# Kernel tuning notes

Measured on AMD Instinct MI355X. Metric: run time of the kernel, lower is better.

## Reference

```python
import jax, jax.numpy as jnp
import numpy as np

N = 10000      # nodes
E = 100000     # edges
H = 256        # hidden_dim
HEADS = 4
HD = H // HEADS
G = 8          # graphs in batch
SPG = N // G   # nodes per graph (equal-size graphs -> to_dense_batch is a reshape)
IN = 16        # in_dim
PE = 5         # pe_dims
ED = 8         # edge_dim
OUT = 4        # out_dim
L = 5          # num_layers


def setup_inputs() -> dict:
    key = jax.random.key(0)
    ks = iter(jax.random.split(key, 64))
    rn = lambda shape, s=0.05: jax.random.normal(next(ks), shape, jnp.float32) * s
    inp = {}
    inp['x'] = jax.random.normal(next(ks), (N, IN), jnp.float32)
    inp['pe'] = jax.random.normal(next(ks), (N, PE), jnp.float32)
    inp['edge_attr'] = jax.random.normal(next(ks), (E, ED), jnp.float32)
    inp['edge_index'] = jax.random.randint(next(ks), (2, E), 0, N, jnp.int32)
    inp['batch'] = (jnp.arange(N) // SPG).astype(jnp.int32)
    # node encoders (3 node types), stacked
    inp['enc_w1'] = rn((3, IN + PE, H)); inp['enc_b1'] = rn((3, H))
    inp['enc_w2'] = rn((3, H, H));       inp['enc_b2'] = rn((3, H))
    # edge encoder
    inp['ee_w1'] = rn((ED, H)); inp['ee_b1'] = rn((H,))
    inp['ee_w2'] = rn((H, H));  inp['ee_b2'] = rn((H,))
    # per-layer edge / node update MLPs, stacked over layers
    inp['eu_w1'] = rn((L, 3 * H, H)); inp['eu_b1'] = rn((L, H))
    inp['eu_w2'] = rn((L, H, H));     inp['eu_b2'] = rn((L, H))
    inp['nu_w1'] = rn((L, 2 * H, H)); inp['nu_b1'] = rn((L, H))
    inp['nu_w2'] = rn((L, H, H));     inp['nu_b2'] = rn((L, H))
    # MultiheadAttention (combined in-proj + out-proj)
    inp['qkv_w'] = rn((H, 3 * H)); inp['qkv_b'] = rn((3 * H,))
    inp['out_w'] = rn((H, H));     inp['out_b'] = rn((H,))
    # fusion MLP
    inp['fu_w1'] = rn((H, H)); inp['fu_b1'] = rn((H,))
    inp['fu_w2'] = rn((H, H)); inp['fu_b2'] = rn((H,))
    # decoders (3 node types)
    inp['dec_w1'] = rn((3, H, H));   inp['dec_b1'] = rn((3, H))
    inp['dec_w2'] = rn((3, H, OUT)); inp['dec_b2'] = rn((3, OUT))
    return inp


def _mlp(z, w1, b1, w2, b2):
    return jnp.maximum(z @ w1 + b1, 0.0) @ w2 + b2


def reference(x, pe, edge_attr, edge_index, batch,
              enc_w1, enc_b1, enc_w2, enc_b2,
              ee_w1, ee_b1, ee_w2, ee_b2,
              eu_w1, eu_b1, eu_w2, eu_b2,
              nu_w1, nu_b1, nu_w2, nu_b2,
              qkv_w, qkv_b, out_w, out_b,
              fu_w1, fu_b1, fu_w2, fu_b2,
              dec_w1, dec_b1, dec_w2, dec_b2):
    n = x.shape[0]
    node_types = (jnp.clip(jnp.round(x[:, 2] * 3.0), 1.0, 3.0).astype(jnp.int32) - 1)
    rng_n = jnp.arange(n)

    # node encoding: run all 3 type-MLPs, select per node (masked dispatch in torch)
    inp = jnp.concatenate([x, pe], axis=-1)                       # [N, IN+PE]
    hid = jnp.maximum(jnp.einsum('ni,tih->tnh', inp, enc_w1) + enc_b1[:, None, :], 0.0)
    h_all = jnp.einsum('tnh,tho->tno', hid, enc_w2) + enc_b2[:, None, :]  # [3,N,H]
    h_nodes = h_all[node_types, rng_n]                            # [N, H]

    h_edges = _mlp(edge_attr, ee_w1, ee_b1, ee_w2, ee_b2)         # [E, H]

    src, dst = edge_index[0], edge_index[1]
    for l in range(L):
        e_in = jnp.concatenate([h_nodes[src], h_nodes[dst], h_edges], axis=-1)  # [E,3H]
        h_edges = h_edges + _mlp(e_in, eu_w1[l], eu_b1[l], eu_w2[l], eu_b2[l])
        m_node = jax.ops.segment_sum(h_edges, dst, num_segments=n)              # index_add_
        n_in = jnp.concatenate([h_nodes, m_node], axis=-1)                      # [N,2H]
        h_nodes = h_nodes + _mlp(n_in, nu_w1[l], nu_b1[l], nu_w2[l], nu_b2[l])

    # global attention: equal-size graphs -> to_dense_batch is a reshape, mask all-true
    xp = h_nodes.reshape(G, SPG, H)
    qkv = xp @ qkv_w + qkv_b                                      # [G,S,3H]
    q, k, v = jnp.split(qkv, 3, axis=-1)
    split_heads = lambda t: t.reshape(G, SPG, HEADS, HD).transpose(0, 2, 1, 3)
    q, k, v = split_heads(q), split_heads(k), split_heads(v)
    scale = 1.0 / np.sqrt(HD).astype(np.float32)
    att = jax.nn.softmax(jnp.einsum('ghsd,ghtd->ghst', q, k) * scale, axis=-1)
    o = jnp.einsum('ghst,ghtd->ghsd', att, v).transpose(0, 2, 1, 3).reshape(G, SPG, H)
    glob = (xp + (o @ out_w + out_b)).reshape(n, H)

    h = _mlp(h_nodes + glob, fu_w1, fu_b1, fu_w2, fu_b2)

    dhid = jnp.maximum(jnp.einsum('nh,tho->tno', h, dec_w1) + dec_b1[:, None, :], 0.0)
    out_all = jnp.einsum('tno,tok->tnk', dhid, dec_w2) + dec_b2[:, None, :]     # [3,N,OUT]
    return out_all[node_types, rng_n]
```

## Files before the change

kernel.cpp:

```cpp
#include <hip/hip_runtime.h>
#include <hip/hip_bf16.h>
#include <math.h>

#define NN 10000
#define NE 100000
#define SPGc 1250
#define NG 8
#define NL 5
#define ECHK 25000

__device__ __forceinline__ int imin(int a, int b) { return a < b ? a : b; }

__global__ __launch_bounds__(256) void k_types(const float* __restrict__ x, int* __restrict__ types) {
    int i = blockIdx.x * 256 + threadIdx.x;
    if (i < NN) {
        float v = rintf(x[(size_t)i * 16 + 2] * 3.0f);
        v = fminf(fmaxf(v, 1.0f), 3.0f);
        types[i] = (int)v - 1;
    }
}

__global__ __launch_bounds__(256) void k_hist(const int* __restrict__ dst, int* __restrict__ deg) {
    int e = blockIdx.x * 256 + threadIdx.x;
    if (e < NE) atomicAdd(&deg[dst[e]], 1);
}

__global__ __launch_bounds__(256) void k_scan(const int* __restrict__ deg, int* __restrict__ row_ptr,
                                              int* __restrict__ cursor) {
    __shared__ int buf[256];
    int tid = threadIdx.x;
    int base = 0;
    for (int c = 0; c < NN; c += 256) {
        int i = c + tid;
        int v = (i < NN) ? deg[i] : 0;
        buf[tid] = v;
        __syncthreads();
        for (int off = 1; off < 256; off <<= 1) {
            int t = (tid >= off) ? buf[tid - off] : 0;
            __syncthreads();
            buf[tid] += t;
            __syncthreads();
        }
        if (i < NN) {
            row_ptr[i + 1] = base + buf[tid];
            cursor[i] = base + buf[tid] - v;
        }
        __syncthreads();
        base += buf[255];
        __syncthreads();
    }
    if (tid == 0) row_ptr[0] = 0;
}

__global__ __launch_bounds__(256) void k_scatter(const int* __restrict__ dst, int* __restrict__ cursor,
                                                 int* __restrict__ csr) {
    int e = blockIdx.x * 256 + threadIdx.x;
    if (e < NE) {
        int p = atomicAdd(&cursor[dst[e]], 1);
        csr[p] = e;
    }
}

__global__ __launch_bounds__(256) void k_enc(const float* __restrict__ x, const float* __restrict__ pe,
        const int* __restrict__ types,
        const float* __restrict__ w1, const float* __restrict__ b1,
        const float* __restrict__ w2, const float* __restrict__ b2,
        float* __restrict__ h_nodes) {
    int n = blockIdx.x;
    int j = threadIdx.x;
    __shared__ float inp[21];
    __shared__ float hid[256];
    if (j < 16) inp[j] = x[(size_t)n * 16 + j];
    else if (j < 21) inp[j] = pe[(size_t)n * 5 + (j - 16)];
    __syncthreads();
    int t = types[n];
    const float* W1 = w1 + (size_t)t * 21 * 256;
    float a = b1[t * 256 + j];
    #pragma unroll
    for (int i = 0; i < 21; ++i) a = fmaf(inp[i], W1[i * 256 + j], a);
    hid[j] = fmaxf(a, 0.f);
    __syncthreads();
    const float* W2 = w2 + (size_t)t * 256 * 256;
    float o = b2[t * 256 + j];
    for (int k = 0; k < 256; ++k) o = fmaf(hid[k], W2[k * 256 + j], o);
    h_nodes[(size_t)n * 256 + j] = o;
}

__global__ __launch_bounds__(256) void gemm64(int Mrows, int K, int Nout,
        const float* __restrict__ A0, int lda,
        const float* __restrict__ W, const float* __restrict__ bias,
        float* __restrict__ C) {
    __shared__ __align__(16) float As[16][68];
    __shared__ __align__(16) float Ws[16][64];
    int tid = threadIdx.x;
    int tx = tid & 15, ty = tid >> 4;
    int blockRow = blockIdx.x * 64;
    int ncol0 = blockIdx.y * 64;
    float acc[4][4];
    #pragma unroll
    for (int i = 0; i < 4; ++i)
        #pragma unroll
        for (int j = 0; j < 4; ++j) acc[i][j] = 0.f;

    for (int k0 = 0; k0 < K; k0 += 16) {
        #pragma unroll
        for (int i = 0; i < 4; ++i) {
            int id = tid + 256 * i;
            int kk = id & 15, r = id >> 4;
            int grow = blockRow + r;
            int k = k0 + kk;
            float v = 0.f;
            if (grow < Mrows && k < K) v = A0[(size_t)grow * lda + k];
            As[kk][r] = v;
        }
        #pragma unroll
        for (int i = 0; i < 4; ++i) {
            int id = tid + 256 * i;
            int c = id & 63, kk = id >> 6;
            int k = k0 + kk;
            Ws[kk][c] = (k < K) ? W[(size_t)k * Nout + ncol0 + c] : 0.f;
        }
        __syncthreads();
        #pragma unroll
        for (int kk = 0; kk < 16; ++kk) {
            const float4 a4 = *(const float4*)&As[kk][ty << 2];
            const float4 w4 = *(const float4*)&Ws[kk][tx << 2];
            float av[4] = {a4.x, a4.y, a4.z, a4.w};
            float wv[4] = {w4.x, w4.y, w4.z, w4.w};
            #pragma unroll
            for (int i = 0; i < 4; ++i)
                #pragma unroll
                for (int j = 0; j < 4; ++j)
                    acc[i][j] = fmaf(av[i], wv[j], acc[i][j]);
        }
        __syncthreads();
    }
    #pragma unroll
    for (int i = 0; i < 4; ++i) {
        int grow = blockRow + (ty << 2) + i;
        if (grow >= Mrows) continue;
        size_t base = (size_t)grow * Nout + ncol0 + (tx << 2);
        #pragma unroll
        for (int j = 0; j < 4; ++j)
            C[base + j] = fmaxf(acc[i][j] + bias[ncol0 + (tx << 2) + j], 0.f);
    }
}

template<int AMODE, bool RELU, bool HASRES, bool PGATH, bool HASBIAS>
__global__ __launch_bounds__(256) void gemm_f32(int Mrows, int K, int Nout,
        const float* __restrict__ A0, const float* __restrict__ A1, int lda, int rowOfsA,
        const int* __restrict__ gsrc, const int* __restrict__ gdst,
        const float* __restrict__ Pa, const float* __restrict__ Pb,
        const float* __restrict__ W, const float* __restrict__ bias,
        const float* __restrict__ ResF, float resScale, int rowOfsC,
        float* __restrict__ C) {
    __shared__ __align__(16) float As[16][68];
    __shared__ __align__(16) float Ws[16][16][20];
    int tid = threadIdx.x;
    int blockRow = blockIdx.x * 64;
    int ncol0 = blockIdx.y * 256;
    int r4 = tid >> 4, c16 = tid & 15;
    int sar = tid >> 2, sak = (tid & 3) * 4;
    int swk = tid >> 4, scg = tid & 15;
    float acc[4][16];
    #pragma unroll
    for (int i = 0; i < 4; ++i)
        #pragma unroll
        for (int n = 0; n < 16; ++n) acc[i][n] = 0.f;

    for (int k0 = 0; k0 < K; k0 += 16) {
        {
            int arow = imin(blockRow + sar, Mrows - 1) + rowOfsA;
            float4 av;
            if (AMODE == 0) {
                av = *(const float4*)(A0 + (size_t)arow * lda + k0 + sak);
            } else {
                int k = k0 + sak;
                av = (k < 256) ? *(const float4*)(A0 + (size_t)arow * 256 + k)
                               : *(const float4*)(A1 + (size_t)arow * 256 + (k - 256));
            }
            As[sak + 0][sar] = av.x;
            As[sak + 1][sar] = av.y;
            As[sak + 2][sar] = av.z;
            As[sak + 3][sar] = av.w;
        }
        {
            const float* wp = W + (size_t)(k0 + swk) * Nout + ncol0 + scg * 16;
            *(float4*)&Ws[swk][scg][0]  = *(const float4*)(wp + 0);
            *(float4*)&Ws[swk][scg][4]  = *(const float4*)(wp + 4);
            *(float4*)&Ws[swk][scg][8]  = *(const float4*)(wp + 8);
            *(float4*)&Ws[swk][scg][12] = *(const float4*)(wp + 12);
        }
        __syncthreads();
        #pragma unroll
        for (int kk = 0; kk < 16; ++kk) {
            const float4 a4 = *(const float4*)&As[kk][r4 << 2];
            float av[4] = {a4.x, a4.y, a4.z, a4.w};
            #pragma unroll
            for (int q = 0; q < 4; ++q) {
                const float4 w4 = *(const float4*)&Ws[kk][c16][q << 2];
                float wv[4] = {w4.x, w4.y, w4.z, w4.w};
                #pragma unroll
                for (int i = 0; i < 4; ++i)
                    #pragma unroll
                    for (int j = 0; j < 4; ++j)
                        acc[i][q * 4 + j] = fmaf(av[i], wv[j], acc[i][q * 4 + j]);
            }
        }
        __syncthreads();
    }
    #pragma unroll
    for (int i = 0; i < 4; ++i) {
        int grow = blockRow + (r4 << 2) + i;
        if (grow >= Mrows) continue;
        size_t crow = (size_t)(grow + rowOfsC);
        int colb = ncol0 + (c16 << 4);
        const float* par = nullptr;
        const float* pbr = nullptr;
        if (PGATH) {
            int e = grow + rowOfsA;
            par = Pa + (size_t)gsrc[e] * 256 + colb;
            pbr = Pb + (size_t)gdst[e] * 256 + colb;
        }
        #pragma unroll
        for (int q = 0; q < 4; ++q) {
            float v[4];
            #pragma unroll
            for (int j = 0; j < 4; ++j) v[j] = acc[i][q * 4 + j];
            if (HASBIAS) {
                const float4 b4 = *(const float4*)(bias + colb + q * 4);
                v[0] += b4.x; v[1] += b4.y; v[2] += b4.z; v[3] += b4.w;
            }
            if (PGATH) {
                const float4 pa4 = *(const float4*)(par + q * 4);
                const float4 pb4 = *(const float4*)(pbr + q * 4);
                v[0] += pa4.x + pb4.x; v[1] += pa4.y + pb4.y;
                v[2] += pa4.z + pb4.z; v[3] += pa4.w + pb4.w;
            }
            if (RELU) {
                v[0] = fmaxf(v[0], 0.f); v[1] = fmaxf(v[1], 0.f);
                v[2] = fmaxf(v[2], 0.f); v[3] = fmaxf(v[3], 0.f);
            }
            if (HASRES) {
                const float4 rv = *(const float4*)(ResF + crow * Nout + colb + q * 4);
                v[0] += resScale * rv.x; v[1] += resScale * rv.y;
                v[2] += resScale * rv.z; v[3] += resScale * rv.w;
            }
            float4 o; o.x = v[0]; o.y = v[1]; o.z = v[2]; o.w = v[3];
            *(float4*)(C + crow * Nout + colb + q * 4) = o;
        }
    }
}

__global__ __launch_bounds__(256) void k_mnode(const float* __restrict__ h_edges,
        const int* __restrict__ row_ptr, const int* __restrict__ csr, float* __restrict__ m_node) {
    int n = blockIdx.x * 4 + (threadIdx.x >> 6);
    int lane = threadIdx.x & 63;
    if (n >= NN) return;
    float a0 = 0.f, a1 = 0.f, a2 = 0.f, a3 = 0.f;
    int s = row_ptr[n], e = row_ptr[n + 1];
    for (int i = s; i < e; ++i) {
        int ed = csr[i];
        const float4 v = *(const float4*)(h_edges + (size_t)ed * 256 + (lane << 2));
        a0 += v.x; a1 += v.y; a2 += v.z; a3 += v.w;
    }
    float4 r; r.x = a0; r.y = a1; r.z = a2; r.w = a3;
    *(float4*)(m_node + (size_t)n * 256 + (lane << 2)) = r;
}

__global__ __launch_bounds__(256) void k_attn(const float* __restrict__ qkv, float* __restrict__ obuf) {
    int gh = blockIdx.y;
    int g = gh >> 2, h = gh & 3;
    int q0 = blockIdx.x * 64;
    int tid = threadIdx.x;
    int r = tid >> 2, q4 = tid & 3;
    int d0 = q4 * 16;
    __shared__ __align__(16) float Ks[32][64];
    __shared__ __align__(16) float Vs[32][64];
    const float* base = qkv + (size_t)g * SPGc * 768;
    int my_s = q0 + r;
    bool rowok = my_s < SPGc;
    float qreg[16];
    #pragma unroll
    for (int dd = 0; dd < 16; ++dd) qreg[dd] = 0.f;
    if (rowok) {
        const float* qp = base + (size_t)my_s * 768 + h * 64 + d0;
        #pragma unroll
        for (int dd = 0; dd < 16; ++dd) qreg[dd] = qp[dd];
    }
    float m = -1e30f, l = 0.f;
    float oacc[16];
    #pragma unroll
    for (int dd = 0; dd < 16; ++dd) oacc[dd] = 0.f;

    for (int t0 = 0; t0 < SPGc; t0 += 32) {
        #pragma unroll
        for (int i = 0; i < 8; ++i) {
            int id = tid + 256 * i;
            int d = id & 63, jj = id >> 6;
            int s = t0 + jj;
            float kv = 0.f, vv = 0.f;
            if (s < SPGc) {
                const float* kp = base + (size_t)s * 768 + h * 64;
                kv = kp[256 + d];
                vv = kp[512 + d];
            }
            Ks[jj][d] = kv;
            Vs[jj][d] = vv;
        }
        __syncthreads();
        float sc[32];
        #pragma unroll
        for (int j = 0; j < 32; ++j) {
            float p = 0.f;
            #pragma unroll
            for (int dd = 0; dd < 16; dd += 4) {
                const float4 k4 = *(const float4*)&Ks[j][d0 + dd];
                p = fmaf(qreg[dd], k4.x, p);
                p = fmaf(qreg[dd + 1], k4.y, p);
                p = fmaf(qreg[dd + 2], k4.z, p);
                p = fmaf(qreg[dd + 3], k4.w, p);
            }
            sc[j] = p;
        }
        #pragma unroll
        for (int j = 0; j < 32; ++j) {
            float p = sc[j];
            p += __shfl_xor(p, 1);
            p += __shfl_xor(p, 2);
            sc[j] = (t0 + j < SPGc) ? p * 0.125f : -1e30f;
        }
        float mt = sc[0];
        #pragma unroll
        for (int j = 1; j < 32; ++j) mt = fmaxf(mt, sc[j]);
        float mnew = fmaxf(m, mt);
        float f = __expf(m - mnew);
        l *= f;
        #pragma unroll
        for (int dd = 0; dd < 16; ++dd) oacc[dd] *= f;
        #pragma unroll
        for (int j = 0; j < 32; ++j) {
            float p = __expf(sc[j] - mnew);
            l += p;
            #pragma unroll
            for (int dd = 0; dd < 16; dd += 4) {
                const float4 v4 = *(const float4*)&Vs[j][d0 + dd];
                oacc[dd]     = fmaf(p, v4.x, oacc[dd]);
                oacc[dd + 1] = fmaf(p, v4.y, oacc[dd + 1]);
                oacc[dd + 2] = fmaf(p, v4.z, oacc[dd + 2]);
                oacc[dd + 3] = fmaf(p, v4.w, oacc[dd + 3]);
            }
        }
        m = mnew;
        __syncthreads();
    }
    if (rowok) {
        float rinv = 1.0f / l;
        float* op = obuf + (size_t)(g * SPGc + my_s) * 256 + h * 64 + d0;
        #pragma unroll
        for (int dd = 0; dd < 16; ++dd) op[dd] = oacc[dd] * rinv;
    }
}

__global__ __launch_bounds__(256) void k_dec(const float* __restrict__ h, const int* __restrict__ types,
        const float* __restrict__ w1, const float* __restrict__ b1,
        const float* __restrict__ w2, const float* __restrict__ b2,
        float* __restrict__ out) {
    int n = blockIdx.x;
    int j = threadIdx.x;
    __shared__ float hrow[256];
    __shared__ float dhid[256];
    hrow[j] = h[(size_t)n * 256 + j];
    __syncthreads();
    int t = types[n];
    const float* W1 = w1 + (size_t)t * 256 * 256;
    float a = b1[t * 256 + j];
    for (int k = 0; k < 256; ++k) a = fmaf(hrow[k], W1[k * 256 + j], a);
    dhid[j] = fmaxf(a, 0.f);
    __syncthreads();
    int lane = j & 63, w = j >> 6;
    const float* W2 = w2 + (size_t)t * 256 * 4;
    float p = 0.f;
    #pragma unroll
    for (int q = 0; q < 4; ++q) {
        int kk = lane + 64 * q;
        p = fmaf(dhid[kk], W2[kk * 4 + w], p);
    }
    #pragma unroll
    for (int o2 = 32; o2 > 0; o2 >>= 1) p += __shfl_down(p, o2);
    if (lane == 0) out[(size_t)n * 4 + w] = p + b2[t * 4 + w];
}

extern "C" void kernel_launch(void* const* d_in, const int* in_sizes, int n_in,
                              void* d_out, int out_size, void* d_ws, size_t ws_size,
                              hipStream_t stream) {
    const float* x         = (const float*)d_in[0];
    const float* pe        = (const float*)d_in[1];
    const float* edge_attr = (const float*)d_in[2];
    const int*   eidx      = (const int*)d_in[3];
    const float* enc_w1 = (const float*)d_in[5];
    const float* enc_b1 = (const float*)d_in[6];
    const float* enc_w2 = (const float*)d_in[7];
    const float* enc_b2 = (const float*)d_in[8];
    const float* ee_w1  = (const float*)d_in[9];
    const float* ee_b1  = (const float*)d_in[10];
    const float* ee_w2  = (const float*)d_in[11];
    const float* ee_b2  = (const float*)d_in[12];
    const float* eu_w1  = (const float*)d_in[13];
    const float* eu_b1  = (const float*)d_in[14];
    const float* eu_w2  = (const float*)d_in[15];
    const float* eu_b2  = (const float*)d_in[16];
    const float* nu_w1  = (const float*)d_in[17];
    const float* nu_b1  = (const float*)d_in[18];
    const float* nu_w2  = (const float*)d_in[19];
    const float* nu_b2  = (const float*)d_in[20];
    const float* qkv_w  = (const float*)d_in[21];
    const float* qkv_b  = (const float*)d_in[22];
    const float* out_w  = (const float*)d_in[23];
    const float* out_b  = (const float*)d_in[24];
    const float* fu_w1  = (const float*)d_in[25];
    const float* fu_b1  = (const float*)d_in[26];
    const float* fu_w2  = (const float*)d_in[27];
    const float* fu_b2  = (const float*)d_in[28];
    const float* dec_w1 = (const float*)d_in[29];
    const float* dec_b1 = (const float*)d_in[30];
    const float* dec_w2 = (const float*)d_in[31];
    const float* dec_b2 = (const float*)d_in[32];

    const int* src  = eidx;
    const int* dstp = eidx + NE;

    float* ws = (float*)d_ws;
    float* h_edges = ws;
    float* big     = ws + 25600000;
    float* h_nodes = ws + 37120000;
    float* mn_ob   = ws + 39680000;
    float* nhid    = ws + 42240000;
    int* ibase   = (int*)(ws + 44800000);
    int* types   = ibase;
    int* deg     = ibase + NN;
    int* row_ptr = deg + NN;
    int* cursor  = row_ptr + NN + 1;
    int* csr     = cursor + NN;

    float* ehid = big;
    float* Pa   = big + 6400000;
    float* Pb   = big + 8960000;
    float* qkvf = big;
    float* fin  = big + 7680000;

    hipMemsetAsync(deg, 0, NN * sizeof(int), stream);
    k_types<<<(NN + 255) / 256, 256, 0, stream>>>(x, types);
    k_hist<<<(NE + 255) / 256, 256, 0, stream>>>(dstp, deg);
    k_scan<<<1, 256, 0, stream>>>(deg, row_ptr, cursor);
    k_scatter<<<(NE + 255) / 256, 256, 0, stream>>>(dstp, cursor, csr);

    k_enc<<<NN, 256, 0, stream>>>(x, pe, types, enc_w1, enc_b1, enc_w2, enc_b2, h_nodes);

    dim3 gE((ECHK + 63) / 64, 1);
    dim3 gN((NN + 63) / 64, 1);

    for (int c0 = 0; c0 < NE; c0 += ECHK) {
        gemm64<<<dim3((ECHK + 63) / 64, 4), 256, 0, stream>>>(ECHK, 8, 256,
            edge_attr + (size_t)c0 * 8, 8, ee_w1, ee_b1, ehid);
        gemm_f32<0, false, false, false, true><<<gE, 256, 0, stream>>>(ECHK, 256, 256,
            ehid, nullptr, 256, 0, nullptr, nullptr, nullptr, nullptr,
            ee_w2, ee_b2, nullptr, 0.f, c0, h_edges);
    }

    for (int l = 0; l < NL; ++l) {
        const float* W1 = eu_w1 + (size_t)l * 768 * 256;
        gemm_f32<0, false, false, false, false><<<gN, 256, 0, stream>>>(NN, 256, 256,
            h_nodes, nullptr, 256, 0, nullptr, nullptr, nullptr, nullptr,
            W1, nullptr, nullptr, 0.f, 0, Pa);
        gemm_f32<0, false, false, false, false><<<gN, 256, 0, stream>>>(NN, 256, 256,
            h_nodes, nullptr, 256, 0, nullptr, nullptr, nullptr, nullptr,
            W1 + 65536, nullptr, nullptr, 0.f, 0, Pb);
        for (int c0 = 0; c0 < NE; c0 += ECHK) {
            gemm_f32<0, true, false, true, true><<<gE, 256, 0, stream>>>(ECHK, 256, 256,
                h_edges, nullptr, 256, c0, src, dstp, Pa, Pb,
                W1 + 131072, eu_b1 + l * 256, nullptr, 0.f, 0, ehid);
            gemm_f32<0, false, true, false, true><<<gE, 256, 0, stream>>>(ECHK, 256, 256,
                ehid, nullptr, 256, 0, nullptr, nullptr, nullptr, nullptr,
                eu_w2 + (size_t)l * 65536, eu_b2 + l * 256, h_edges, 1.f, c0, h_edges);
        }
        k_mnode<<<(NN + 3) / 4, 256, 0, stream>>>(h_edges, row_ptr, csr, mn_ob);
        gemm_f32<2, true, false, false, true><<<gN, 256, 0, stream>>>(NN, 512, 256,
            h_nodes, mn_ob, 256, 0, nullptr, nullptr, nullptr, nullptr,
            nu_w1 + (size_t)l * 131072, nu_b1 + l * 256, nullptr, 0.f, 0, nhid);
        gemm_f32<0, false, true, false, true><<<gN, 256, 0, stream>>>(NN, 256, 256,
            nhid, nullptr, 256, 0, nullptr, nullptr, nullptr, nullptr,
            nu_w2 + (size_t)l * 65536, nu_b2 + l * 256, h_nodes, 1.f, 0, h_nodes);
    }

    gemm_f32<0, false, false, false, true><<<dim3((NN + 63) / 64, 3), 256, 0, stream>>>(NN, 256, 768,
        h_nodes, nullptr, 256, 0, nullptr, nullptr, nullptr, nullptr,
        qkv_w, qkv_b, nullptr, 0.f, 0, qkvf);

    dim3 ga((SPGc + 63) / 64, NG * 4);
    k_attn<<<ga, 256, 0, stream>>>(qkvf, mn_ob);

    gemm_f32<0, false, true, false, true><<<gN, 256, 0, stream>>>(NN, 256, 256,
        mn_ob, nullptr, 256, 0, nullptr, nullptr, nullptr, nullptr,
        out_w, out_b, h_nodes, 2.f, 0, fin);
    gemm_f32<0, true, false, false, true><<<gN, 256, 0, stream>>>(NN, 256, 256,
        fin, nullptr, 256, 0, nullptr, nullptr, nullptr, nullptr,
        fu_w1, fu_b1, nullptr, 0.f, 0, nhid);
    gemm_f32<0, false, false, false, true><<<gN, 256, 0, stream>>>(NN, 256, 256,
        nhid, nullptr, 256, 0, nullptr, nullptr, nullptr, nullptr,
        fu_w2, fu_b2, nullptr, 0.f, 0, mn_ob);

    k_dec<<<NN, 256, 0, stream>>>(mn_ob, types, dec_w1, dec_b1, dec_w2, dec_b2, (float*)d_out);
}
```

Before: 4.436 ms.

## Fuse edge MLP into one kernel keeping hidden tile in LDS, narrow node GEMM tiles

```diff
diff --git a/kernel.cpp b/kernel.cpp
--- a/kernel.cpp
+++ b/kernel.cpp
@@ -7,7 +7,6 @@
 #define SPGc 1250
 #define NG 8
 #define NL 5
-#define ECHK 25000
 
 __device__ __forceinline__ int imin(int a, int b) { return a < b ? a : b; }
 
@@ -82,95 +81,165 @@
     __syncthreads();
     const float* W2 = w2 + (size_t)t * 256 * 256;
     float o = b2[t * 256 + j];
+    #pragma unroll 8
     for (int k = 0; k < 256; ++k) o = fmaf(hid[k], W2[k * 256 + j], o);
     h_nodes[(size_t)n * 256 + j] = o;
 }
 
-__global__ __launch_bounds__(256) void gemm64(int Mrows, int K, int Nout,
-        const float* __restrict__ A0, int lda,
+template<bool GATHER, bool RES>
+__global__ __launch_bounds__(256) void k_eu(int Mrows, int K1,
+        const float* __restrict__ A, int lda,
+        const float* __restrict__ W1, const float* __restrict__ b1,
+        const int* __restrict__ gs, const int* __restrict__ gd,
+        const float* __restrict__ Pa, const float* __restrict__ Pb,
+        const float* __restrict__ W2, const float* __restrict__ b2,
+        float* __restrict__ HE) {
+    __shared__ __align__(16) float E[256][65];
+    __shared__ __align__(16) float As[8][68];
+    __shared__ __align__(16) float Ws[8][16][20];
+    int tid = threadIdx.x;
+    int blockRow = blockIdx.x * 64;
+    int rg = tid >> 4, cg = tid & 15;
+    float acc[4][16];
+    #pragma unroll
+    for (int i = 0; i < 4; ++i)
+        #pragma unroll
+        for (int n = 0; n < 16; ++n) acc[i][n] = 0.f;
+
+    for (int k0 = 0; k0 < K1; k0 += 8) {
+        {
+            int row = tid & 63, kh = tid >> 6;
+            int arow = imin(blockRow + row, Mrows - 1);
+            const float* ap = A + (size_t)arow * lda + k0 + kh * 2;
+            float2 a2 = *(const float2*)ap;
+            As[kh * 2][row] = a2.x;
+            As[kh * 2 + 1][row] = a2.y;
+        }
+        {
+            int kk = tid >> 5, cgw = (tid >> 1) & 15, half = tid & 1;
+            const float* wp = W1 + (size_t)(k0 + kk) * 256 + cgw * 16 + half * 8;
+            float4 w0 = *(const float4*)wp;
+            float4 w1 = *(const float4*)(wp + 4);
+            *(float4*)&Ws[kk][cgw][half * 8]     = w0;
+            *(float4*)&Ws[kk][cgw][half * 8 + 4] = w1;
+        }
+        __syncthreads();
+        #pragma unroll
+        for (int kk = 0; kk < 8; ++kk) {
+            const float4 a4 = *(const float4*)&As[kk][rg << 2];
+            float av[4] = {a4.x, a4.y, a4.z, a4.w};
+            #pragma unroll
+            for (int q = 0; q < 4; ++q) {
+                const float4 w4 = *(const float4*)&Ws[kk][cg][q << 2];
+                float wv[4] = {w4.x, w4.y, w4.z, w4.w};
+                #pragma unroll
+                for (int i = 0; i < 4; ++i)
+                    #pragma unroll
+                    for (int j = 0; j < 4; ++j)
+                        acc[i][q * 4 + j] = fmaf(av[i], wv[j], acc[i][q * 4 + j]);
+            }
+        }
+        __syncthreads();
+    }
+    int gsi[4], gdi[4];
+    if (GATHER) {
+        #pragma unroll
+        for (int i = 0; i < 4; ++i) {
+            int e = imin(blockRow + (rg << 2) + i, Mrows - 1);
+            gsi[i] = gs[e];
+            gdi[i] = gd[e];
+        }
+    }
+    #pragma unroll
+    for (int n = 0; n < 16; ++n) {
+        int col = (cg << 4) + n;
+        float bv = b1[col];
+        float4 w;
+        float* wf = (float*)&w;
+        #pragma unroll
+        for (int i = 0; i < 4; ++i) {
+            float v = acc[i][n] + bv;
+            if (GATHER) v += Pa[(size_t)gsi[i] * 256 + col] + Pb[(size_t)gdi[i] * 256 + col];
+            wf[i] = fmaxf(v, 0.f);
+        }
+        *(float4*)&E[col][rg << 2] = w;
+    }
+    #pragma unroll
+    for (int i = 0; i < 4; ++i)
+        #pragma unroll
+        for (int n = 0; n < 16; ++n) acc[i][n] = 0.f;
+    __syncthreads();
+
+    for (int k0 = 0; k0 < 256; k0 += 8) {
+        {
+            int kk = tid >> 5, cgw = (tid >> 1) & 15, half = tid & 1;
+            const float* wp = W2 + (size_t)(k0 + kk) * 256 + cgw * 16 + half * 8;
+            float4 w0 = *(const float4*)wp;
+            float4 w1 = *(const float4*)(wp + 4);
+            *(float4*)&Ws[kk][cgw][half * 8]     = w0;
+            *(float4*)&Ws[kk][cgw][half * 8 + 4] = w1;
+        }
+        __syncthreads();
+        #pragma unroll
+        for (int kk = 0; kk < 8; ++kk) {
+            const float4 a4 = *(const float4*)&E[k0 + kk][rg << 2];
+            float av[4] = {a4.x, a4.y, a4.z, a4.w};
+            #pragma unroll
+            for (int q = 0; q < 4; ++q) {
+                const float4 w4 = *(const float4*)&Ws[kk][cg][q << 2];
+                float wv[4] = {w4.x, w4.y, w4.z, w4.w};
+                #pragma unroll
+                for (int i = 0; i < 4; ++i)
+                    #pragma unroll
+                    for (int j = 0; j < 4; ++j)
+                        acc[i][q * 4 + j] = fmaf(av[i], wv[j], acc[i][q * 4 + j]);
+            }
+        }
+        __syncthreads();
+    }
+    #pragma unroll
+    for (int i = 0; i < 4; ++i) {
+        int row = blockRow + (rg << 2) + i;
+        if (row >= Mrows) continue;
+        size_t base = (size_t)row * 256 + (cg << 4);
+        #pragma unroll
+        for (int q = 0; q < 4; ++q) {
+            const float4 b4 = *(const float4*)(b2 + (cg << 4) + q * 4);
+            float v[4] = {acc[i][q * 4 + 0] + b4.x, acc[i][q * 4 + 1] + b4.y,
+                          acc[i][q * 4 + 2] + b4.z, acc[i][q * 4 + 3] + b4.w};
+            if (RES) {
+                const float4 rv = *(const float4*)(HE + base + q * 4);
+                v[0] += rv.x; v[1] += rv.y; v[2] += rv.z; v[3] += rv.w;
+            }
+            float4 o; o.x = v[0]; o.y = v[1]; o.z = v[2]; o.w = v[3];
+            *(float4*)(HE + base + q * 4) = o;
+        }
+    }
+}
+
+template<int AMODE, bool RELU, bool HASRES, bool HASBIAS>
+__global__ __launch_bounds__(256) void gemm_f32(int Mrows, int K, int Nout,
+        const float* __restrict__ A0, const float* __restrict__ A1, int lda,
         const float* __restrict__ W, const float* __restrict__ bias,
+        const float* __restrict__ ResF, float resScale,
         float* __restrict__ C) {
     __shared__ __align__(16) float As[16][68];
-    __shared__ __align__(16) float Ws[16][64];
-    int tid = threadIdx.x;
-    int tx = tid & 15, ty = tid >> 4;
-    int blockRow = blockIdx.x * 64;
-    int ncol0 = blockIdx.y * 64;
-    float acc[4][4];
-    #pragma unroll
-    for (int i = 0; i < 4; ++i)
-        #pragma unroll
-        for (int j = 0; j < 4; ++j) acc[i][j] = 0.f;
-
-    for (int k0 = 0; k0 < K; k0 += 16) {
-        #pragma unroll
-        for (int i = 0; i < 4; ++i) {
-            int id = tid + 256 * i;
-            int kk = id & 15, r = id >> 4;
-            int grow = blockRow + r;
-            int k = k0 + kk;
-            float v = 0.f;
-            if (grow < Mrows && k < K) v = A0[(size_t)grow * lda + k];
-            As[kk][r] = v;
-        }
-        #pragma unroll
-        for (int i = 0; i < 4; ++i) {
-            int id = tid + 256 * i;
-            int c = id & 63, kk = id >> 6;
-            int k = k0 + kk;
-            Ws[kk][c] = (k < K) ? W[(size_t)k * Nout + ncol0 + c] : 0.f;
-        }
-        __syncthreads();
-        #pragma unroll
-        for (int kk = 0; kk < 16; ++kk) {
-            const float4 a4 = *(const float4*)&As[kk][ty << 2];
-            const float4 w4 = *(const float4*)&Ws[kk][tx << 2];
-            float av[4] = {a4.x, a4.y, a4.z, a4.w};
-            float wv[4] = {w4.x, w4.y, w4.z, w4.w};
-            #pragma unroll
-            for (int i = 0; i < 4; ++i)
-                #pragma unroll
-                for (int j = 0; j < 4; ++j)
-                    acc[i][j] = fmaf(av[i], wv[j], acc[i][j]);
-        }
-        __syncthreads();
-    }
-    #pragma unroll
-    for (int i = 0; i < 4; ++i) {
-        int grow = blockRow + (ty << 2) + i;
-        if (grow >= Mrows) continue;
-        size_t base = (size_t)grow * Nout + ncol0 + (tx << 2);
-        #pragma unroll
-        for (int j = 0; j < 4; ++j)
-            C[base + j] = fmaxf(acc[i][j] + bias[ncol0 + (tx << 2) + j], 0.f);
-    }
-}
-
-template<int AMODE, bool RELU, bool HASRES, bool PGATH, bool HASBIAS>
-__global__ __launch_bounds__(256) void gemm_f32(int Mrows, int K, int Nout,
-        const float* __restrict__ A0, const float* __restrict__ A1, int lda, int rowOfsA,
-        const int* __restrict__ gsrc, const int* __restrict__ gdst,
-        const float* __restrict__ Pa, const float* __restrict__ Pb,
-        const float* __restrict__ W, const float* __restrict__ bias,
-        const float* __restrict__ ResF, float resScale, int rowOfsC,
-        float* __restrict__ C) {
-    __shared__ __align__(16) float As[16][68];
-    __shared__ __align__(16) float Ws[16][16][20];
+    __shared__ __align__(16) float Ws[16][16][10];
     int tid = threadIdx.x;
     int blockRow = blockIdx.x * 64;
-    int ncol0 = blockIdx.y * 256;
-    int r4 = tid >> 4, c16 = tid & 15;
+    int ncol0 = blockIdx.y * 128;
+    int rg = tid >> 4, cg = tid & 15;
     int sar = tid >> 2, sak = (tid & 3) * 4;
     int swk = tid >> 4, scg = tid & 15;
-    float acc[4][16];
+    float acc[4][8];
     #pragma unroll
     for (int i = 0; i < 4; ++i)
         #pragma unroll
-        for (int n = 0; n < 16; ++n) acc[i][n] = 0.f;
+        for (int n = 0; n < 8; ++n) acc[i][n] = 0.f;
 
     for (int k0 = 0; k0 < K; k0 += 16) {
         {
-            int arow = imin(blockRow + sar, Mrows - 1) + rowOfsA;
+            int arow = imin(blockRow + sar, Mrows - 1);
             float4 av;
             if (AMODE == 0) {
                 av = *(const float4*)(A0 + (size_t)arow * lda + k0 + sak);
@@ -185,57 +254,40 @@
             As[sak + 3][sar] = av.w;
         }
         {
-            const float* wp = W + (size_t)(k0 + swk) * Nout + ncol0 + scg * 16;
-            *(float4*)&Ws[swk][scg][0]  = *(const float4*)(wp + 0);
-            *(float4*)&Ws[swk][scg][4]  = *(const float4*)(wp + 4);
-            *(float4*)&Ws[swk][scg][8]  = *(const float4*)(wp + 8);
-            *(float4*)&Ws[swk][scg][12] = *(const float4*)(wp + 12);
+            const float* wp = W + (size_t)(k0 + swk) * Nout + ncol0 + scg * 8;
+            *(float4*)&Ws[swk][scg][0] = *(const float4*)(wp + 0);
+            *(float4*)&Ws[swk][scg][4] = *(const float4*)(wp + 4);
         }
         __syncthreads();
         #pragma unroll
         for (int kk = 0; kk < 16; ++kk) {
-            const float4 a4 = *(const float4*)&As[kk][r4 << 2];
+            const float4 a4 = *(const float4*)&As[kk][rg << 2];
             float av[4] = {a4.x, a4.y, a4.z, a4.w};
+            const float4 w0 = *(const float4*)&Ws[kk][cg][0];
+            const float4 w1 = *(const float4*)&Ws[kk][cg][4];
+            float wv[8] = {w0.x, w0.y, w0.z, w0.w, w1.x, w1.y, w1.z, w1.w};
             #pragma unroll
-            for (int q = 0; q < 4; ++q) {
-                const float4 w4 = *(const float4*)&Ws[kk][c16][q << 2];
-                float wv[4] = {w4.x, w4.y, w4.z, w4.w};
+            for (int i = 0; i < 4; ++i)
                 #pragma unroll
-                for (int i = 0; i < 4; ++i)
-                    #pragma unroll
-                    for (int j = 0; j < 4; ++j)
-                        acc[i][q * 4 + j] = fmaf(av[i], wv[j], acc[i][q * 4 + j]);
-            }
+                for (int j = 0; j < 8; ++j)
+                    acc[i][j] = fmaf(av[i], wv[j], acc[i][j]);
         }
         __syncthreads();
     }
     #pragma unroll
     for (int i = 0; i < 4; ++i) {
-        int grow = blockRow + (r4 << 2) + i;
+        int grow = blockRow + (rg << 2) + i;
         if (grow >= Mrows) continue;
-        size_t crow = (size_t)(grow + rowOfsC);
-        int colb = ncol0 + (c16 << 4);
-        const float* par = nullptr;
-        const float* pbr = nullptr;
-        if (PGATH) {
-            int e = grow + rowOfsA;
-            par = Pa + (size_t)gsrc[e] * 256 + colb;
-            pbr = Pb + (size_t)gdst[e] * 256 + colb;
-        }
-        #pragma unroll
-        for (int q = 0; q < 4; ++q) {
+        size_t crow = (size_t)grow;
+        int colb = ncol0 + (cg << 3);
+        #pragma unroll
+        for (int q = 0; q < 2; ++q) {
             float v[4];
             #pragma unroll
             for (int j = 0; j < 4; ++j) v[j] = acc[i][q * 4 + j];
             if (HASBIAS) {
                 const float4 b4 = *(const float4*)(bias + colb + q * 4);
                 v[0] += b4.x; v[1] += b4.y; v[2] += b4.z; v[3] += b4.w;
-            }
-            if (PGATH) {
-                const float4 pa4 = *(const float4*)(par + q * 4);
-                const float4 pb4 = *(const float4*)(pbr + q * 4);
-                v[0] += pa4.x + pb4.x; v[1] += pa4.y + pb4.y;
-                v[2] += pa4.z + pb4.z; v[3] += pa4.w + pb4.w;
             }
             if (RELU) {
                 v[0] = fmaxf(v[0], 0.f); v[1] = fmaxf(v[1], 0.f);
@@ -275,8 +327,8 @@
     int tid = threadIdx.x;
     int r = tid >> 2, q4 = tid & 3;
     int d0 = q4 * 16;
-    __shared__ __align__(16) float Ks[32][64];
-    __shared__ __align__(16) float Vs[32][64];
+    __shared__ __align__(16) float Ks[32][68];
+    __shared__ __align__(16) float Vs[32][68];
     const float* base = qkv + (size_t)g * SPGc * 768;
     int my_s = q0 + r;
     bool rowok = my_s < SPGc;
@@ -293,20 +345,22 @@
     #pragma unroll
     for (int dd = 0; dd < 16; ++dd) oacc[dd] = 0.f;
 
+    int srow = tid >> 3, sc8 = (tid & 7) * 8;
     for (int t0 = 0; t0 < SPGc; t0 += 32) {
-        #pragma unroll
-        for (int i = 0; i < 8; ++i) {
-            int id = tid + 256 * i;
-            int d = id & 63, jj = id >> 6;
-            int s = t0 + jj;
-            float kv = 0.f, vv = 0.f;
+        {
+            int s = t0 + srow;
+            float4 k0v = {0,0,0,0}, k1v = {0,0,0,0}, v0v = {0,0,0,0}, v1v = {0,0,0,0};
             if (s < SPGc) {
-                const float* kp = base + (size_t)s * 768 + h * 64;
-                kv = kp[256 + d];
-                vv = kp[512 + d];
-            }
-            Ks[jj][d] = kv;
-            Vs[jj][d] = vv;
+                const float* kp = base + (size_t)s * 768 + h * 64 + sc8;
+                k0v = *(const float4*)(kp + 256);
+                k1v = *(const float4*)(kp + 260);
+                v0v = *(const float4*)(kp + 512);
+                v1v = *(const float4*)(kp + 516);
+            }
+            *(float4*)&Ks[srow][sc8]     = k0v;
+            *(float4*)&Ks[srow][sc8 + 4] = k1v;
+            *(float4*)&Vs[srow][sc8]     = v0v;
+            *(float4*)&Vs[srow][sc8 + 4] = v1v;
         }
         __syncthreads();
         float sc[32];
@@ -375,6 +429,7 @@
     int t = types[n];
     const float* W1 = w1 + (size_t)t * 256 * 256;
     float a = b1[t * 256 + j];
+    #pragma unroll 8
     for (int k = 0; k < 256; ++k) a = fmaf(hrow[k], W1[k * 256 + j], a);
     dhid[j] = fmaxf(a, 0.f);
     __syncthreads();
@@ -432,22 +487,21 @@
 
     float* ws = (float*)d_ws;
     float* h_edges = ws;
-    float* big     = ws + 25600000;
-    float* h_nodes = ws + 37120000;
-    float* mn_ob   = ws + 39680000;
-    float* nhid    = ws + 42240000;
-    int* ibase   = (int*)(ws + 44800000);
+    float* region  = ws + 25600000;
+    float* h_nodes = ws + 33280000;
+    float* mn_ob   = ws + 35840000;
+    float* nhid    = ws + 38400000;
+    int* ibase   = (int*)(ws + 40960000);
     int* types   = ibase;
     int* deg     = ibase + NN;
     int* row_ptr = deg + NN;
     int* cursor  = row_ptr + NN + 1;
     int* csr     = cursor + NN;
 
-    float* ehid = big;
-    float* Pa   = big + 6400000;
-    float* Pb   = big + 8960000;
-    float* qkvf = big;
-    float* fin  = big + 7680000;
+    float* Pa   = region;
+    float* Pb   = region + 2560000;
+    float* qkvf = region;
+    float* fin  = region;
 
     hipMemsetAsync(deg, 0, NN * sizeof(int), stream);
     k_types<<<(NN + 255) / 256, 256, 0, stream>>>(x, types);
@@ -457,58 +511,42 @@
 
     k_enc<<<NN, 256, 0, stream>>>(x, pe, types, enc_w1, enc_b1, enc_w2, enc_b2, h_nodes);
 
-    dim3 gE((ECHK + 63) / 64, 1);
-    dim3 gN((NN + 63) / 64, 1);
-
-    for (int c0 = 0; c0 < NE; c0 += ECHK) {
-        gemm64<<<dim3((ECHK + 63) / 64, 4), 256, 0, stream>>>(ECHK, 8, 256,
-            edge_attr + (size_t)c0 * 8, 8, ee_w1, ee_b1, ehid);
-        gemm_f32<0, false, false, false, true><<<gE, 256, 0, stream>>>(ECHK, 256, 256,
-            ehid, nullptr, 256, 0, nullptr, nullptr, nullptr, nullptr,
-            ee_w2, ee_b2, nullptr, 0.f, c0, h_edges);
-    }
+    int gEU = (NE + 63) / 64;
+    dim3 gN((NN + 63) / 64, 2);
+
+    k_eu<false, false><<<gEU, 256, 0, stream>>>(NE, 8, edge_attr, 8,
+        ee_w1, ee_b1, nullptr, nullptr, nullptr, nullptr, ee_w2, ee_b2, h_edges);
 
     for (int l = 0; l < NL; ++l) {
         const float* W1 = eu_w1 + (size_t)l * 768 * 256;
-        gemm_f32<0, false, false, false, false><<<gN, 256, 0, stream>>>(NN, 256, 256,
-            h_nodes, nullptr, 256, 0, nullptr, nullptr, nullptr, nullptr,
-            W1, nullptr, nullptr, 0.f, 0, Pa);
-        gemm_f32<0, false, false, false, false><<<gN, 256, 0, stream>>>(NN, 256, 256,
-            h_nodes, nullptr, 256, 0, nullptr, nullptr, nullptr, nullptr,
-            W1 + 65536, nullptr, nullptr, 0.f, 0, Pb);
-        for (int c0 = 0; c0 < NE; c0 += ECHK) {
-            gemm_f32<0, true, false, true, true><<<gE, 256, 0, stream>>>(ECHK, 256, 256,
-                h_edges, nullptr, 256, c0, src, dstp, Pa, Pb,
-                W1 + 131072, eu_b1 + l * 256, nullptr, 0.f, 0, ehid);
-            gemm_f32<0, false, true, false, true><<<gE, 256, 0, stream>>>(ECHK, 256, 256,
-                ehid, nullptr, 256, 0, nullptr, nullptr, nullptr, nullptr,
-                eu_w2 + (size_t)l * 65536, eu_b2 + l * 256, h_edges, 1.f, c0, h_edges);
-        }
+        gemm_f32<0, false, false, false><<<gN, 256, 0, stream>>>(NN, 256, 256,
+            h_nodes, nullptr, 256, W1, nullptr, nullptr, 0.f, Pa);
+        gemm_f32<0, false, false, false><<<gN, 256, 0, stream>>>(NN, 256, 256,
+            h_nodes, nullptr, 256, W1 + 65536, nullptr, nullptr, 0.f, Pb);
+        k_eu<true, true><<<gEU, 256, 0, stream>>>(NE, 256, h_edges, 256,
+            W1 + 131072, eu_b1 + l * 256, src, dstp, Pa, Pb,
+            eu_w2 + (size_t)l * 65536, eu_b2 + l * 256, h_edges);
         k_mnode<<<(NN + 3) / 4, 256, 0, stream>>>(h_edges, row_ptr, csr, mn_ob);
-        gemm_f32<2, true, false, false, true><<<gN, 256, 0, stream>>>(NN, 512, 256,
-            h_nodes, mn_ob, 256, 0, nullptr, nullptr, nullptr, nullptr,
-            nu_w1 + (size_t)l * 131072, nu_b1 + l * 256, nullptr, 0.f, 0, nhid);
-        gemm_f32<0, false, true, false, true><<<gN, 256, 0, stream>>>(NN, 256, 256,
-            nhid, nullptr, 256, 0, nullptr, nullptr, nullptr, nullptr,
-            nu_w2 + (size_t)l * 65536, nu_b2 + l * 256, h_nodes, 1.f, 0, h_nodes);
-    }
-
-    gemm_f32<0, false, false, false, true><<<dim3((NN + 63) / 64, 3), 256, 0, stream>>>(NN, 256, 768,
-        h_nodes, nullptr, 256, 0, nullptr, nullptr, nullptr, nullptr,
-        qkv_w, qkv_b, nullptr, 0.f, 0, qkvf);
+        gemm_f32<2, true, false, true><<<gN, 256, 0, stream>>>(NN, 512, 256,
+            h_nodes, mn_ob, 256, nu_w1 + (size_t)l * 131072, nu_b1 + l * 256,
+            nullptr, 0.f, nhid);
+        gemm_f32<0, false, true, true><<<gN, 256, 0, stream>>>(NN, 256, 256,
+            nhid, nullptr, 256, nu_w2 + (size_t)l * 65536, nu_b2 + l * 256,
+            h_nodes, 1.f, h_nodes);
+    }
+
+    gemm_f32<0, false, false, true><<<dim3((NN + 63) / 64, 6), 256, 0, stream>>>(NN, 256, 768,
+        h_nodes, nullptr, 256, qkv_w, qkv_b, nullptr, 0.f, qkvf);
 
     dim3 ga((SPGc + 63) / 64, NG * 4);
     k_attn<<<ga, 256, 0, stream>>>(qkvf, mn_ob);
 
-    gemm_f32<0, false, true, false, true><<<gN, 256, 0, stream>>>(NN, 256, 256,
-        mn_ob, nullptr, 256, 0, nullptr, nullptr, nullptr, nullptr,
-        out_w, out_b, h_nodes, 2.f, 0, fin);
-    gemm_f32<0, true, false, false, true><<<gN, 256, 0, stream>>>(NN, 256, 256,
-        fin, nullptr, 256, 0, nullptr, nullptr, nullptr, nullptr,
-        fu_w1, fu_b1, nullptr, 0.f, 0, nhid);
-    gemm_f32<0, false, false, false, true><<<gN, 256, 0, stream>>>(NN, 256, 256,
-        nhid, nullptr, 256, 0, nullptr, nullptr, nullptr, nullptr,
-        fu_w2, fu_b2, nullptr, 0.f, 0, mn_ob);
+    gemm_f32<0, false, true, true><<<gN, 256, 0, stream>>>(NN, 256, 256,
+        mn_ob, nullptr, 256, out_w, out_b, h_nodes, 2.f, fin);
+    gemm_f32<0, true, false, true><<<gN, 256, 0, stream>>>(NN, 256, 256,
+        fin, nullptr, 256, fu_w1, fu_b1, nullptr, 0.f, nhid);
+    gemm_f32<0, false, false, true><<<gN, 256, 0, stream>>>(NN, 256, 256,
+        nhid, nullptr, 256, fu_w2, fu_b2, nullptr, 0.f, mn_ob);
 
     k_dec<<<NN, 256, 0, stream>>>(mn_ob, types, dec_w1, dec_b1, dec_w2, dec_b2, (float*)d_out);
 }
```

After: 5.120 ms. 1.15x slower.
